# Performance work log

Measured on AMD Instinct MI355X. Metric: run time of the kernel, lower is better.

The kernel has to match this reference:

```python
import jax, jax.numpy as jnp
import numpy as np

N = 20000       # nodes
E = 640000      # random edges (self-loops appended -> E + N total)
G = 64          # graphs in batch
F_IN = 114
H1 = 3          # heads in layer 1
D2 = 128        # output_dim of layer 2
NEG = 0.2       # GATConv leaky_relu negative slope


def setup_inputs() -> dict:
    key = jax.random.key(0)
    ks = jax.random.split(key, 20)
    x = jax.random.normal(ks[0], (N, F_IN), jnp.float32)
    src = jax.random.randint(ks[1], (E,), 0, N, jnp.int32)
    dst = jax.random.randint(ks[2], (E,), 0, N, jnp.int32)
    loop = jnp.arange(N, dtype=jnp.int32)  # PyG add_self_loops=True
    edge_index = jnp.stack([jnp.concatenate([src, loop]),
                            jnp.concatenate([dst, loop])])
    batch = (jnp.arange(N) * G // N).astype(jnp.int32)  # every graph non-empty

    def lin(k, i, o):
        return jax.random.normal(k, (i, o), jnp.float32) * (1.0 / np.sqrt(i))

    return {
        "x": x, "edge_index": edge_index, "batch": batch,
        # GATConv 1: 114 -> 114 per head, 3 heads, concat
        "W1": lin(ks[3], F_IN, H1 * F_IN),
        "a_src1": jax.random.normal(ks[4], (H1, F_IN), jnp.float32) * 0.1,
        "a_dst1": jax.random.normal(ks[5], (H1, F_IN), jnp.float32) * 0.1,
        "b1": jnp.zeros((H1 * F_IN,), jnp.float32),
        # GATConv 2: 342 -> 128, 1 head
        "W2": lin(ks[6], H1 * F_IN, D2),
        "a_src2": jax.random.normal(ks[7], (1, D2), jnp.float32) * 0.1,
        "a_dst2": jax.random.normal(ks[8], (1, D2), jnp.float32) * 0.1,
        "b2": jnp.zeros((D2,), jnp.float32),
        # MLP head
        "Wg": lin(ks[9], D2, 64),  "bg": jnp.zeros((64,), jnp.float32),
        "Wf1": lin(ks[10], 64, 32), "bf1": jnp.zeros((32,), jnp.float32),
        "Wf2": lin(ks[11], 32, 16), "bf2": jnp.zeros((16,), jnp.float32),
        "Wo": lin(ks[12], 16, 1),   "bo": jnp.zeros((1,), jnp.float32),
    }


def gat_conv(x, edge_index, W, a_src, a_dst, b, heads, dim):
    """PyG GATConv (self-loops already in edge_index, eval mode)."""
    n = x.shape[0]
    h = (x @ W).reshape(n, heads, dim)             # [N,H,D]
    src, dst = edge_index[0], edge_index[1]
    alpha_s = jnp.sum(h * a_src, axis=-1)          # [N,H]
    alpha_d = jnp.sum(h * a_dst, axis=-1)          # [N,H]
    e = jax.nn.leaky_relu(alpha_s[src] + alpha_d[dst], NEG)  # [E,H]
    # segment softmax over destination nodes
    m = jax.ops.segment_max(e, dst, num_segments=n)
    ex = jnp.exp(e - m[dst])
    s = jax.ops.segment_sum(ex, dst, num_segments=n)
    alpha = ex / s[dst]                            # [E,H]
    out = jax.ops.segment_sum(h[src] * alpha[..., None], dst, num_segments=n)
    return out.reshape(n, heads * dim) + b


def reference(x, edge_index, batch, W1, a_src1, a_dst1, b1,
              W2, a_src2, a_dst2, b2, Wg, bg, Wf1, bf1, Wf2, bf2, Wo, bo):
    h = jax.nn.elu(gat_conv(x, edge_index, W1, a_src1, a_dst1, b1, H1, F_IN))
    h = jax.nn.relu(gat_conv(h, edge_index, W2, a_src2, a_dst2, b2, 1, D2))
    g = jax.ops.segment_max(h, batch, num_segments=G)   # global max pool [G,128]
    g = jax.nn.relu(g @ Wg + bg)
    g = jax.nn.relu(g @ Wf1 + bf1)
    g = jax.nn.relu(g @ Wf2 + bf2)
    return g @ Wo + bo                                  # [G,1]
```

## Files before the change

kernel.cpp:

```cpp
#include <hip/hip_runtime.h>

#define NN 20000
#define EE 660000
#define GG 64
#define FIN 114
#define H1 3
#define F1 342
#define D2 128
#define NEG 0.2f

typedef __attribute__((ext_vector_type(8))) short short8v;
typedef __attribute__((ext_vector_type(4))) float f32x4;
typedef unsigned short ushort_t;

__device__ inline unsigned fenc(float f) {
    unsigned u = __float_as_uint(f);
    return (u & 0x80000000u) ? ~u : (u | 0x80000000u);
}
__device__ inline float fdec(unsigned u) {
    return (u & 0x80000000u) ? __uint_as_float(u & 0x7FFFFFFFu) : __uint_as_float(~u);
}
__device__ inline float lrelu(float x) { return x > 0.f ? x : NEG * x; }

__device__ inline void split2(float x, ushort_t& hi, ushort_t& lo) {
    unsigned u = __float_as_uint(x);
    unsigned uh = u & 0xFFFF0000u;
    hi = (ushort_t)(uh >> 16);
    float r = x - __uint_as_float(uh);
    unsigned v = __float_as_uint(r);
    unsigned vh = (v + 0x7FFFu + ((v >> 16) & 1u)) & 0xFFFF0000u;
    lo = (ushort_t)(vh >> 16);
}

__global__ void k_wa(const float* __restrict__ W1, const float* __restrict__ aS,
                     const float* __restrict__ aD, float* __restrict__ was,
                     float* __restrict__ wad) {
    int tid = blockIdx.x * 256 + threadIdx.x;
    if (tid >= 2 * FIN * H1) return;
    int which = tid >= FIN * H1;
    int i = which ? tid - FIN * H1 : tid;
    int k = i / H1, h = i % H1;
    const float* a = which ? aD : aS;
    float s = 0.f;
    for (int d = 0; d < FIN; d++) s += W1[k * F1 + h * FIN + d] * a[h * FIN + d];
    (which ? wad : was)[i] = s;
}

__global__ void k_prep1m(const float* __restrict__ W1, ushort_t* __restrict__ W1Th,
                         ushort_t* __restrict__ W1Tl) {
    int tid = blockIdx.x * 256 + threadIdx.x;
    if (tid >= H1 * 128 * 128) return;
    int h = tid / (128 * 128);
    int rem = tid & (128 * 128 - 1);
    int c = rem >> 7, k = rem & 127;
    float v = (c < FIN && k < FIN) ? W1[k * F1 + h * FIN + c] : 0.f;
    ushort_t hi, lo;
    split2(v, hi, lo);
    W1Th[tid] = hi;
    W1Tl[tid] = lo;
}

__global__ void k_prep2m(const float* __restrict__ W2, ushort_t* __restrict__ W2Th,
                         ushort_t* __restrict__ W2Tl) {
    int tid = blockIdx.x * 256 + threadIdx.x;
    if (tid >= 128 * 384) return;
    int c = tid / 384;
    int hk = tid - c * 384;
    int h = hk >> 7, k = hk & 127;
    float v = (k < FIN) ? W2[(h * FIN + k) * D2 + c] : 0.f;
    ushort_t hi, lo;
    split2(v, hi, lo);
    W2Th[tid] = hi;
    W2Tl[tid] = lo;
}

__global__ __launch_bounds__(256) void k_alpha1x(const float* __restrict__ x,
                                                 const float* __restrict__ was,
                                                 const float* __restrict__ wad,
                                                 float* __restrict__ as1,
                                                 float* __restrict__ ad1) {
    int n = blockIdx.x * 4 + (threadIdx.x >> 6);
    int l = threadIdx.x & 63;
    if (n >= NN) return;
    float x0 = x[n * FIN + l];
    float x1 = (l < FIN - 64) ? x[n * FIN + 64 + l] : 0.f;
    float s[H1], d[H1];
#pragma unroll
    for (int h = 0; h < H1; h++) {
        float w0s = was[l * H1 + h], w0d = wad[l * H1 + h];
        float w1s = (l < FIN - 64) ? was[(64 + l) * H1 + h] : 0.f;
        float w1d = (l < FIN - 64) ? wad[(64 + l) * H1 + h] : 0.f;
        s[h] = x0 * w0s + x1 * w1s;
        d[h] = x0 * w0d + x1 * w1d;
    }
#pragma unroll
    for (int o = 32; o > 0; o >>= 1) {
#pragma unroll
        for (int h = 0; h < H1; h++) {
            s[h] += __shfl_down(s[h], o);
            d[h] += __shfl_down(d[h], o);
        }
    }
    if (l == 0) {
#pragma unroll
        for (int h = 0; h < H1; h++) {
            as1[n * H1 + h] = s[h];
            ad1[n * H1 + h] = d[h];
        }
    }
}

__global__ void k_count(const int* __restrict__ dst, int* __restrict__ cnt) {
    int e = blockIdx.x * 256 + threadIdx.x;
    if (e < EE) atomicAdd(&cnt[dst[e]], 1);
}

__global__ __launch_bounds__(1024) void k_scan(const int* __restrict__ cnt,
                                               int* __restrict__ off) {
    __shared__ int part[1024];
    int t = threadIdx.x;
    const int CH = 20;
    int loc[CH];
    int s = 0;
    int base = t * CH;
    for (int i = 0; i < CH; i++) {
        int idx = base + i;
        int v = (idx < NN) ? cnt[idx] : 0;
        loc[i] = s;
        s += v;
    }
    part[t] = s;
    __syncthreads();
    for (int d = 1; d < 1024; d <<= 1) {
        int v = (t >= d) ? part[t - d] : 0;
        __syncthreads();
        part[t] += v;
        __syncthreads();
    }
    int pre = (t == 0) ? 0 : part[t - 1];
    for (int i = 0; i < CH; i++) {
        int idx = base + i;
        if (idx < NN) off[idx] = pre + loc[i];
    }
    if (t == 1023) off[NN] = part[1023];
}

__global__ void k_scatter(const int* __restrict__ src, const int* __restrict__ dst,
                          const int* __restrict__ off, int* __restrict__ cur,
                          int* __restrict__ csr_src) {
    int e = blockIdx.x * 256 + threadIdx.x;
    if (e < EE) {
        int d = dst[e];
        int pos = off[d] + atomicAdd(&cur[d], 1);
        csr_src[pos] = src[e];
    }
}

__global__ __launch_bounds__(128) void k_aggx(const float* __restrict__ x,
                                              const float* __restrict__ as1,
                                              const float* __restrict__ ad1,
                                              const int* __restrict__ off,
                                              const int* __restrict__ csr_src,
                                              ushort_t* __restrict__ xgh,
                                              ushort_t* __restrict__ xgl) {
    int n = blockIdx.x, t = threadIdx.x;
    int e0 = off[n], e1 = off[n + 1];
    float adv0 = ad1[n * H1 + 0], adv1 = ad1[n * H1 + 1], adv2 = ad1[n * H1 + 2];
    __shared__ int ssrc[64];
    __shared__ float sw[64][H1];
    __shared__ float red[64][H1];
    float acc0 = 0.f, acc1 = 0.f, acc2 = 0.f;
    float ps0 = 0.f, ps1 = 0.f, ps2 = 0.f;
    for (int base = e0; base < e1; base += 64) {
        int c = min(64, e1 - base);
        __syncthreads();
        if (t < c) {
            int s = csr_src[base + t];
            ssrc[t] = s;
            float w0 = __expf(lrelu(as1[s * H1 + 0] + adv0));
            float w1 = __expf(lrelu(as1[s * H1 + 1] + adv1));
            float w2 = __expf(lrelu(as1[s * H1 + 2] + adv2));
            sw[t][0] = w0; sw[t][1] = w1; sw[t][2] = w2;
            ps0 += w0; ps1 += w1; ps2 += w2;
        }
        __syncthreads();
        if (t < FIN) {
            for (int j = 0; j < c; j++) {
                float xv = x[ssrc[j] * FIN + t];
                acc0 += xv * sw[j][0];
                acc1 += xv * sw[j][1];
                acc2 += xv * sw[j][2];
            }
        }
    }
    __syncthreads();
    if (t < 64) { red[t][0] = ps0; red[t][1] = ps1; red[t][2] = ps2; }
    __syncthreads();
    for (int sr = 32; sr > 0; sr >>= 1) {
        if (t < sr) {
            red[t][0] += red[t + sr][0];
            red[t][1] += red[t + sr][1];
            red[t][2] += red[t + sr][2];
        }
        __syncthreads();
    }
    float i0 = 1.f / red[0][0], i1 = 1.f / red[0][1], i2 = 1.f / red[0][2];
    float v0 = (t < FIN) ? acc0 * i0 : 0.f;
    float v1 = (t < FIN) ? acc1 * i1 : 0.f;
    float v2 = (t < FIN) ? acc2 * i2 : 0.f;
    ushort_t hi, lo;
    split2(v0, hi, lo);
    xgh[(size_t)0 * NN * 128 + n * 128 + t] = hi;
    xgl[(size_t)0 * NN * 128 + n * 128 + t] = lo;
    split2(v1, hi, lo);
    xgh[(size_t)1 * NN * 128 + n * 128 + t] = hi;
    xgl[(size_t)1 * NN * 128 + n * 128 + t] = lo;
    split2(v2, hi, lo);
    xgh[(size_t)2 * NN * 128 + n * 128 + t] = hi;
    xgl[(size_t)2 * NN * 128 + n * 128 + t] = lo;
}

__global__ __launch_bounds__(128) void k_agg2f(const float* __restrict__ h2,
                                               const float* __restrict__ as2,
                                               const float* __restrict__ ad2,
                                               const int* __restrict__ off,
                                               const int* __restrict__ csr_src,
                                               const float* __restrict__ b2,
                                               unsigned* __restrict__ poolbuf) {
    int n = blockIdx.x, t = threadIdx.x;
    int e0 = off[n], e1 = off[n + 1];
    float adv = ad2[n];
    __shared__ int ssrc[64];
    __shared__ float sw[64];
    __shared__ float red[64];
    float acc = 0.f, ps = 0.f;
    for (int base = e0; base < e1; base += 64) {
        int c = min(64, e1 - base);
        __syncthreads();
        if (t < c) {
            int s = csr_src[base + t];
            ssrc[t] = s;
            float w = __expf(lrelu(as2[s] + adv));
            sw[t] = w;
            ps += w;
        }
        __syncthreads();
        for (int j = 0; j < c; j++) acc += h2[(size_t)ssrc[j] * D2 + t] * sw[j];
    }
    __syncthreads();
    if (t < 64) red[t] = ps;
    __syncthreads();
    for (int sr = 32; sr > 0; sr >>= 1) {
        if (t < sr) red[t] += red[t + sr];
        __syncthreads();
    }
    float v = fmaxf(acc / red[0] + b2[t], 0.f);
    int g = (int)(((long long)n * GG) / NN);
    atomicMax(&poolbuf[g * D2 + t], fenc(v));
}

__global__ __launch_bounds__(256) void k_gemm1m(const ushort_t* __restrict__ xgh,
                                                const ushort_t* __restrict__ xgl,
                                                const ushort_t* __restrict__ W1Th,
                                                const ushort_t* __restrict__ W1Tl,
                                                const float* __restrict__ b1,
                                                ushort_t* __restrict__ h1hi,
                                                ushort_t* __restrict__ h1lo) {
    int h = blockIdx.y;
    int rb = blockIdx.x * 128;
    int tid = threadIdx.x;
    int w = tid >> 6, l = tid & 63;
    int m = l & 15, g = l >> 4;
    int r0 = rb + w * 32 + m;
    int r1 = r0 + 16;
    bool ok0 = (r0 < NN), ok1 = (r1 < NN);
    const ushort_t* xh = xgh + (size_t)h * NN * 128;
    const ushort_t* xl = xgl + (size_t)h * NN * 128;
    const ushort_t* Bhg = W1Th + (size_t)h * 128 * 128;
    const ushort_t* Blg = W1Tl + (size_t)h * 128 * 128;
    const short8v z8 = {0, 0, 0, 0, 0, 0, 0, 0};
    __shared__ __align__(16) ushort_t BsH[128 * 40];
    __shared__ __align__(16) ushort_t BsL[128 * 40];
    f32x4 acc0[8], acc1[8];
#pragma unroll
    for (int j = 0; j < 8; j++) {
        acc0[j] = (f32x4){0.f, 0.f, 0.f, 0.f};
        acc1[j] = (f32x4){0.f, 0.f, 0.f, 0.f};
    }
    for (int k0i = 0; k0i < 4; k0i++) {
        int k0 = k0i * 32;
        __syncthreads();
        int ka = k0 + g * 8;
        short8v a0h = ok0 ? *(const short8v*)(xh + (size_t)r0 * 128 + ka) : z8;
        short8v a0l = ok0 ? *(const short8v*)(xl + (size_t)r0 * 128 + ka) : z8;
        short8v a1h = ok1 ? *(const short8v*)(xh + (size_t)r1 * 128 + ka) : z8;
        short8v a1l = ok1 ? *(const short8v*)(xl + (size_t)r1 * 128 + ka) : z8;
#pragma unroll
        for (int it = 0; it < 2; it++) {
            int idx = tid + it * 256;
            int c = idx >> 2, q = idx & 3;
            size_t go = (size_t)c * 128 + k0 + q * 8;
            int lo_off = c * 40 + q * 8;
            *(short8v*)(&BsH[lo_off]) = *(const short8v*)(Bhg + go);
            *(short8v*)(&BsL[lo_off]) = *(const short8v*)(Blg + go);
        }
        __syncthreads();
#pragma unroll
        for (int j = 0; j < 8; j++) {
            int c = j * 16 + m;
            short8v bh = *(const short8v*)(&BsH[c * 40 + g * 8]);
            short8v bl = *(const short8v*)(&BsL[c * 40 + g * 8]);
            acc0[j] = __builtin_amdgcn_mfma_f32_16x16x32_bf16(a0h, bh, acc0[j], 0, 0, 0);
            acc1[j] = __builtin_amdgcn_mfma_f32_16x16x32_bf16(a1h, bh, acc1[j], 0, 0, 0);
            acc0[j] = __builtin_amdgcn_mfma_f32_16x16x32_bf16(a0h, bl, acc0[j], 0, 0, 0);
            acc1[j] = __builtin_amdgcn_mfma_f32_16x16x32_bf16(a1h, bl, acc1[j], 0, 0, 0);
            acc0[j] = __builtin_amdgcn_mfma_f32_16x16x32_bf16(a0l, bh, acc0[j], 0, 0, 0);
            acc1[j] = __builtin_amdgcn_mfma_f32_16x16x32_bf16(a1l, bh, acc1[j], 0, 0, 0);
        }
    }
    ushort_t* Hh = h1hi + (size_t)h * NN * 128;
    ushort_t* Hl = h1lo + (size_t)h * NN * 128;
#pragma unroll
    for (int j = 0; j < 8; j++) {
        int c = j * 16 + m;
        float bv = (c < FIN) ? b1[h * FIN + c] : 0.f;
#pragma unroll
        for (int r = 0; r < 4; r++) {
            int orow0 = rb + w * 32 + g * 4 + r;
            int orow1 = orow0 + 16;
            if (orow0 < NN) {
                float v = acc0[j][r] + bv;
                v = v > 0.f ? v : expm1f(v);
                ushort_t hi = 0, lo = 0;
                if (c < FIN) split2(v, hi, lo);
                Hh[(size_t)orow0 * 128 + c] = hi;
                Hl[(size_t)orow0 * 128 + c] = lo;
            }
            if (orow1 < NN) {
                float v = acc1[j][r] + bv;
                v = v > 0.f ? v : expm1f(v);
                ushort_t hi = 0, lo = 0;
                if (c < FIN) split2(v, hi, lo);
                Hh[(size_t)orow1 * 128 + c] = hi;
                Hl[(size_t)orow1 * 128 + c] = lo;
            }
        }
    }
}

__global__ __launch_bounds__(256) void k_gemm2m(const ushort_t* __restrict__ h1hi,
                                                const ushort_t* __restrict__ h1lo,
                                                const ushort_t* __restrict__ W2Th,
                                                const ushort_t* __restrict__ W2Tl,
                                                float* __restrict__ h2) {
    int rb = blockIdx.x * 128;
    int tid = threadIdx.x;
    int w = tid >> 6, l = tid & 63;
    int m = l & 15, g = l >> 4;
    int r0 = rb + w * 32 + m;
    int r1 = r0 + 16;
    bool ok0 = (r0 < NN), ok1 = (r1 < NN);
    const short8v z8 = {0, 0, 0, 0, 0, 0, 0, 0};
    __shared__ __align__(16) ushort_t BsH[128 * 40];
    __shared__ __align__(16) ushort_t BsL[128 * 40];
    f32x4 acc0[8], acc1[8];
#pragma unroll
    for (int j = 0; j < 8; j++) {
        acc0[j] = (f32x4){0.f, 0.f, 0.f, 0.f};
        acc1[j] = (f32x4){0.f, 0.f, 0.f, 0.f};
    }
    for (int k0i = 0; k0i < 12; k0i++) {
        int k0 = k0i * 32;
        __syncthreads();
        int hh = k0 >> 7;
        int kc = (k0 & 127) + g * 8;
        size_t a0o = ((size_t)hh * NN + (size_t)(ok0 ? r0 : 0)) * 128 + kc;
        size_t a1o = ((size_t)hh * NN + (size_t)(ok1 ? r1 : 0)) * 128 + kc;
        short8v a0h = ok0 ? *(const short8v*)(h1hi + a0o) : z8;
        short8v a0l = ok0 ? *(const short8v*)(h1lo + a0o) : z8;
        short8v a1h = ok1 ? *(const short8v*)(h1hi + a1o) : z8;
        short8v a1l = ok1 ? *(const short8v*)(h1lo + a1o) : z8;
#pragma unroll
        for (int it = 0; it < 2; it++) {
            int idx = tid + it * 256;
            int c = idx >> 2, q = idx & 3;
            size_t go = (size_t)c * 384 + k0 + q * 8;
            int lo_off = c * 40 + q * 8;
            *(short8v*)(&BsH[lo_off]) = *(const short8v*)(W2Th + go);
            *(short8v*)(&BsL[lo_off]) = *(const short8v*)(W2Tl + go);
        }
        __syncthreads();
#pragma unroll
        for (int j = 0; j < 8; j++) {
            int c = j * 16 + m;
            short8v bh = *(const short8v*)(&BsH[c * 40 + g * 8]);
            short8v bl = *(const short8v*)(&BsL[c * 40 + g * 8]);
            acc0[j] = __builtin_amdgcn_mfma_f32_16x16x32_bf16(a0h, bh, acc0[j], 0, 0, 0);
            acc1[j] = __builtin_amdgcn_mfma_f32_16x16x32_bf16(a1h, bh, acc1[j], 0, 0, 0);
            acc0[j] = __builtin_amdgcn_mfma_f32_16x16x32_bf16(a0h, bl, acc0[j], 0, 0, 0);
            acc1[j] = __builtin_amdgcn_mfma_f32_16x16x32_bf16(a1h, bl, acc1[j], 0, 0, 0);
            acc0[j] = __builtin_amdgcn_mfma_f32_16x16x32_bf16(a0l, bh, acc0[j], 0, 0, 0);
            acc1[j] = __builtin_amdgcn_mfma_f32_16x16x32_bf16(a1l, bh, acc1[j], 0, 0, 0);
        }
    }
#pragma unroll
    for (int j = 0; j < 8; j++) {
        int c = j * 16 + m;
#pragma unroll
        for (int r = 0; r < 4; r++) {
            int orow0 = rb + w * 32 + g * 4 + r;
            int orow1 = orow0 + 16;
            if (orow0 < NN) h2[(size_t)orow0 * D2 + c] = acc0[j][r];
            if (orow1 < NN) h2[(size_t)orow1 * D2 + c] = acc1[j][r];
        }
    }
}

__global__ __launch_bounds__(256) void k_alpha2(const float* __restrict__ h2,
                                                const float* __restrict__ aS,
                                                const float* __restrict__ aD,
                                                float* __restrict__ as2,
                                                float* __restrict__ ad2) {
    int n = blockIdx.x * 4 + (threadIdx.x >> 6);
    int l = threadIdx.x & 63;
    if (n >= NN) return;
    float v0 = h2[(size_t)n * D2 + l], v1 = h2[(size_t)n * D2 + 64 + l];
    float ps = v0 * aS[l] + v1 * aS[64 + l];
    float pd = v0 * aD[l] + v1 * aD[64 + l];
    for (int o = 32; o > 0; o >>= 1) {
        ps += __shfl_down(ps, o);
        pd += __shfl_down(pd, o);
    }
    if (l == 0) {
        as2[n] = ps;
        ad2[n] = pd;
    }
}

__global__ __launch_bounds__(128) void k_mlp(const unsigned* __restrict__ poolbuf,
                                             const float* __restrict__ Wg,
                                             const float* __restrict__ bg,
                                             const float* __restrict__ Wf1,
                                             const float* __restrict__ bf1,
                                             const float* __restrict__ Wf2,
                                             const float* __restrict__ bf2,
                                             const float* __restrict__ Wo,
                                             const float* __restrict__ bo,
                                             float* __restrict__ out) {
    int g = blockIdx.x;
    int t = threadIdx.x;
    __shared__ float pool[D2];
    __shared__ float a1[64];
    __shared__ float a2[32];
    __shared__ float a3[16];
    pool[t] = fdec(poolbuf[g * D2 + t]);
    __syncthreads();
    if (t < 64) {
        float acc = bg[t];
        for (int k = 0; k < D2; k++) acc += pool[k] * Wg[k * 64 + t];
        a1[t] = fmaxf(acc, 0.f);
    }
    __syncthreads();
    if (t < 32) {
        float acc = bf1[t];
        for (int k = 0; k < 64; k++) acc += a1[k] * Wf1[k * 32 + t];
        a2[t] = fmaxf(acc, 0.f);
    }
    __syncthreads();
    if (t < 16) {
        float acc = bf2[t];
        for (int k = 0; k < 32; k++) acc += a2[k] * Wf2[k * 16 + t];
        a3[t] = fmaxf(acc, 0.f);
    }
    __syncthreads();
    if (t == 0) {
        float acc = bo[0];
        for (int k = 0; k < 16; k++) acc += a3[k] * Wo[k];
        out[g] = acc;
    }
}

extern "C" void kernel_launch(void* const* d_in, const int* in_sizes, int n_in,
                              void* d_out, int out_size, void* d_ws, size_t ws_size,
                              hipStream_t stream) {
    const float* x = (const float*)d_in[0];
    const int* ei = (const int*)d_in[1];
    const float* W1 = (const float*)d_in[3];
    const float* aS1 = (const float*)d_in[4];
    const float* aD1 = (const float*)d_in[5];
    const float* b1 = (const float*)d_in[6];
    const float* W2 = (const float*)d_in[7];
    const float* aS2 = (const float*)d_in[8];
    const float* aD2 = (const float*)d_in[9];
    const float* b2 = (const float*)d_in[10];
    const float* Wg = (const float*)d_in[11];
    const float* bg = (const float*)d_in[12];
    const float* Wf1 = (const float*)d_in[13];
    const float* bf1 = (const float*)d_in[14];
    const float* Wf2 = (const float*)d_in[15];
    const float* bf2 = (const float*)d_in[16];
    const float* Wo = (const float*)d_in[17];
    const float* bo = (const float*)d_in[18];
    float* out = (float*)d_out;

    const int* src = ei;
    const int* dst = ei + EE;

    char* ws = (char*)d_ws;
    size_t o = 0;
    auto alloc = [&](size_t bytes) -> char* {
        char* p = ws + o;
        o += (bytes + 255) & ~(size_t)255;
        return p;
    };
    float* was = (float*)alloc((size_t)FIN * H1 * 4);
    float* wad = (float*)alloc((size_t)FIN * H1 * 4);
    ushort_t* W1Th = (ushort_t*)alloc((size_t)H1 * 128 * 128 * 2);
    ushort_t* W1Tl = (ushort_t*)alloc((size_t)H1 * 128 * 128 * 2);
    ushort_t* W2Th = (ushort_t*)alloc((size_t)128 * 384 * 2);
    ushort_t* W2Tl = (ushort_t*)alloc((size_t)128 * 384 * 2);
    float* as1 = (float*)alloc((size_t)NN * H1 * 4);
    float* ad1 = (float*)alloc((size_t)NN * H1 * 4);
    int* cnt = (int*)alloc((size_t)NN * 4);
    int* off = (int*)alloc((size_t)(NN + 1) * 4);
    int* cur = (int*)alloc((size_t)NN * 4);
    int* csr_src = (int*)alloc((size_t)EE * 4);
    ushort_t* xgh = (ushort_t*)alloc((size_t)H1 * NN * 128 * 2);
    ushort_t* xgl = (ushort_t*)alloc((size_t)H1 * NN * 128 * 2);
    ushort_t* h1hi = (ushort_t*)alloc((size_t)H1 * NN * 128 * 2);
    ushort_t* h1lo = (ushort_t*)alloc((size_t)H1 * NN * 128 * 2);
    float* h2 = (float*)alloc((size_t)NN * D2 * 4);
    float* as2 = (float*)alloc((size_t)NN * 4);
    float* ad2 = (float*)alloc((size_t)NN * 4);
    unsigned* poolbuf = (unsigned*)alloc((size_t)GG * D2 * 4);
    (void)ws_size;

    hipMemsetAsync(cnt, 0, (size_t)NN * 4, stream);
    hipMemsetAsync(cur, 0, (size_t)NN * 4, stream);
    hipMemsetAsync(poolbuf, 0, (size_t)GG * D2 * 4, stream);

    const int EB = (EE + 255) / 256;

    k_wa<<<(2 * FIN * H1 + 255) / 256, 256, 0, stream>>>(W1, aS1, aD1, was, wad);
    k_prep1m<<<(H1 * 128 * 128 + 255) / 256, 256, 0, stream>>>(W1, W1Th, W1Tl);
    k_prep2m<<<(128 * 384 + 255) / 256, 256, 0, stream>>>(W2, W2Th, W2Tl);
    k_alpha1x<<<(NN + 3) / 4, 256, 0, stream>>>(x, was, wad, as1, ad1);
    k_count<<<EB, 256, 0, stream>>>(dst, cnt);
    k_scan<<<1, 1024, 0, stream>>>(cnt, off);
    k_scatter<<<EB, 256, 0, stream>>>(src, dst, off, cur, csr_src);
    k_aggx<<<NN, 128, 0, stream>>>(x, as1, ad1, off, csr_src, xgh, xgl);
    k_gemm1m<<<dim3((NN + 127) / 128, H1), 256, 0, stream>>>(xgh, xgl, W1Th, W1Tl, b1, h1hi, h1lo);
    k_gemm2m<<<(NN + 127) / 128, 256, 0, stream>>>(h1hi, h1lo, W2Th, W2Tl, h2);
    k_alpha2<<<(NN + 3) / 4, 256, 0, stream>>>(h2, aS2, aD2, as2, ad2);
    k_agg2f<<<NN, 128, 0, stream>>>(h2, as2, ad2, off, csr_src, b2, poolbuf);
    k_mlp<<<GG, 128, 0, stream>>>(poolbuf, Wg, bg, Wf1, bf1, Wf2, bf2, Wo, bo, out);
}
```

Baseline: 278.9 us.

## Vectorize edge aggregation with float4 gathers and fuse alpha2 into GEMM2 epilogue

Both per-node aggregation kernels now split the 128 threads into 4 edge groups, each gathering float4 column chunks, and reduce the partial sums through shared memory. A padded 128-wide copy of x is built first so the layer-1 gathers are aligned and vectorized. The attention-logit computation for layer 2 moves into the GEMM2 epilogue, using shuffle reductions over the accumulators, which removes one kernel and one reread of h2. The cost is an extra padded x buffer and its copy kernel, and more shared-memory reduction work per node.

Result: slower. 324.5 us (+16.3%).

```diff
diff --git a/kernel.cpp b/kernel.cpp
--- a/kernel.cpp
+++ b/kernel.cpp
@@ -12,6 +12,7 @@
 typedef __attribute__((ext_vector_type(8))) short short8v;
 typedef __attribute__((ext_vector_type(4))) float f32x4;
 typedef unsigned short ushort_t;
+typedef __attribute__((ext_vector_type(4))) unsigned short ushort4v;
 
 __device__ inline unsigned fenc(float f) {
     unsigned u = __float_as_uint(f);
@@ -72,6 +73,13 @@
     split2(v, hi, lo);
     W2Th[tid] = hi;
     W2Tl[tid] = lo;
+}
+
+__global__ void k_xp(const float* __restrict__ x, float* __restrict__ xP) {
+    int tid = blockIdx.x * 256 + threadIdx.x;
+    if (tid >= NN * 128) return;
+    int n = tid >> 7, c = tid & 127;
+    xP[tid] = (c < FIN) ? x[n * FIN + c] : 0.f;
 }
 
 __global__ __launch_bounds__(256) void k_alpha1x(const float* __restrict__ x,
@@ -156,7 +164,7 @@
     }
 }
 
-__global__ __launch_bounds__(128) void k_aggx(const float* __restrict__ x,
+__global__ __launch_bounds__(128) void k_aggx(const float* __restrict__ xP,
                                               const float* __restrict__ as1,
                                               const float* __restrict__ ad1,
                                               const int* __restrict__ off,
@@ -164,12 +172,15 @@
                                               ushort_t* __restrict__ xgh,
                                               ushort_t* __restrict__ xgl) {
     int n = blockIdx.x, t = threadIdx.x;
+    int g = t >> 5, c32 = t & 31;
+    int col0 = c32 * 4;
     int e0 = off[n], e1 = off[n + 1];
     float adv0 = ad1[n * H1 + 0], adv1 = ad1[n * H1 + 1], adv2 = ad1[n * H1 + 2];
     __shared__ int ssrc[64];
     __shared__ float sw[64][H1];
-    __shared__ float red[64][H1];
-    float acc0 = 0.f, acc1 = 0.f, acc2 = 0.f;
+    __shared__ f32x4 red[4][32][H1];
+    __shared__ float sums[H1];
+    f32x4 a0 = {0, 0, 0, 0}, a1 = {0, 0, 0, 0}, a2 = {0, 0, 0, 0};
     float ps0 = 0.f, ps1 = 0.f, ps2 = 0.f;
     for (int base = e0; base < e1; base += 64) {
         int c = min(64, e1 - base);
@@ -184,40 +195,48 @@
             ps0 += w0; ps1 += w1; ps2 += w2;
         }
         __syncthreads();
-        if (t < FIN) {
-            for (int j = 0; j < c; j++) {
-                float xv = x[ssrc[j] * FIN + t];
-                acc0 += xv * sw[j][0];
-                acc1 += xv * sw[j][1];
-                acc2 += xv * sw[j][2];
-            }
-        }
-    }
+        for (int j = g; j < c; j += 4) {
+            int s = ssrc[j];
+            f32x4 v = *(const f32x4*)(xP + (size_t)s * 128 + col0);
+            float w0 = sw[j][0], w1 = sw[j][1], w2 = sw[j][2];
+            a0 += v * w0;
+            a1 += v * w1;
+            a2 += v * w2;
+        }
+    }
+    if (t < 64) {
+#pragma unroll
+        for (int o = 32; o > 0; o >>= 1) {
+            ps0 += __shfl_down(ps0, o);
+            ps1 += __shfl_down(ps1, o);
+            ps2 += __shfl_down(ps2, o);
+        }
+        if (t == 0) { sums[0] = ps0; sums[1] = ps1; sums[2] = ps2; }
+    }
+    red[g][c32][0] = a0;
+    red[g][c32][1] = a1;
+    red[g][c32][2] = a2;
     __syncthreads();
-    if (t < 64) { red[t][0] = ps0; red[t][1] = ps1; red[t][2] = ps2; }
-    __syncthreads();
-    for (int sr = 32; sr > 0; sr >>= 1) {
-        if (t < sr) {
-            red[t][0] += red[t + sr][0];
-            red[t][1] += red[t + sr][1];
-            red[t][2] += red[t + sr][2];
-        }
-        __syncthreads();
-    }
-    float i0 = 1.f / red[0][0], i1 = 1.f / red[0][1], i2 = 1.f / red[0][2];
-    float v0 = (t < FIN) ? acc0 * i0 : 0.f;
-    float v1 = (t < FIN) ? acc1 * i1 : 0.f;
-    float v2 = (t < FIN) ? acc2 * i2 : 0.f;
-    ushort_t hi, lo;
-    split2(v0, hi, lo);
-    xgh[(size_t)0 * NN * 128 + n * 128 + t] = hi;
-    xgl[(size_t)0 * NN * 128 + n * 128 + t] = lo;
-    split2(v1, hi, lo);
-    xgh[(size_t)1 * NN * 128 + n * 128 + t] = hi;
-    xgl[(size_t)1 * NN * 128 + n * 128 + t] = lo;
-    split2(v2, hi, lo);
-    xgh[(size_t)2 * NN * 128 + n * 128 + t] = hi;
-    xgl[(size_t)2 * NN * 128 + n * 128 + t] = lo;
+    if (t < 32) {
+        f32x4 r0 = red[0][t][0] + red[1][t][0] + red[2][t][0] + red[3][t][0];
+        f32x4 r1 = red[0][t][1] + red[1][t][1] + red[2][t][1] + red[3][t][1];
+        f32x4 r2 = red[0][t][2] + red[1][t][2] + red[2][t][2] + red[3][t][2];
+        float i0 = 1.f / sums[0], i1 = 1.f / sums[1], i2 = 1.f / sums[2];
+        int cb = t * 4;
+        ushort4v h4, l4;
+#pragma unroll
+        for (int q = 0; q < 4; q++) { ushort_t hh, ll; split2(r0[q] * i0, hh, ll); h4[q] = hh; l4[q] = ll; }
+        *(ushort4v*)(xgh + (size_t)0 * NN * 128 + (size_t)n * 128 + cb) = h4;
+        *(ushort4v*)(xgl + (size_t)0 * NN * 128 + (size_t)n * 128 + cb) = l4;
+#pragma unroll
+        for (int q = 0; q < 4; q++) { ushort_t hh, ll; split2(r1[q] * i1, hh, ll); h4[q] = hh; l4[q] = ll; }
+        *(ushort4v*)(xgh + (size_t)1 * NN * 128 + (size_t)n * 128 + cb) = h4;
+        *(ushort4v*)(xgl + (size_t)1 * NN * 128 + (size_t)n * 128 + cb) = l4;
+#pragma unroll
+        for (int q = 0; q < 4; q++) { ushort_t hh, ll; split2(r2[q] * i2, hh, ll); h4[q] = hh; l4[q] = ll; }
+        *(ushort4v*)(xgh + (size_t)2 * NN * 128 + (size_t)n * 128 + cb) = h4;
+        *(ushort4v*)(xgl + (size_t)2 * NN * 128 + (size_t)n * 128 + cb) = l4;
+    }
 }
 
 __global__ __launch_bounds__(128) void k_agg2f(const float* __restrict__ h2,
@@ -228,12 +247,16 @@
                                                const float* __restrict__ b2,
                                                unsigned* __restrict__ poolbuf) {
     int n = blockIdx.x, t = threadIdx.x;
+    int g = t >> 5, c32 = t & 31;
+    int col0 = c32 * 4;
     int e0 = off[n], e1 = off[n + 1];
     float adv = ad2[n];
     __shared__ int ssrc[64];
     __shared__ float sw[64];
-    __shared__ float red[64];
-    float acc = 0.f, ps = 0.f;
+    __shared__ f32x4 red[4][32];
+    __shared__ float ssum;
+    f32x4 acc = {0, 0, 0, 0};
+    float ps = 0.f;
     for (int base = e0; base < e1; base += 64) {
         int c = min(64, e1 - base);
         __syncthreads();
@@ -245,18 +268,29 @@
             ps += w;
         }
         __syncthreads();
-        for (int j = 0; j < c; j++) acc += h2[(size_t)ssrc[j] * D2 + t] * sw[j];
-    }
+        for (int j = g; j < c; j += 4) {
+            f32x4 v = *(const f32x4*)(h2 + (size_t)ssrc[j] * D2 + col0);
+            acc += v * sw[j];
+        }
+    }
+    if (t < 64) {
+#pragma unroll
+        for (int o = 32; o > 0; o >>= 1) ps += __shfl_down(ps, o);
+        if (t == 0) ssum = ps;
+    }
+    red[g][c32] = acc;
     __syncthreads();
-    if (t < 64) red[t] = ps;
-    __syncthreads();
-    for (int sr = 32; sr > 0; sr >>= 1) {
-        if (t < sr) red[t] += red[t + sr];
-        __syncthreads();
-    }
-    float v = fmaxf(acc / red[0] + b2[t], 0.f);
-    int g = (int)(((long long)n * GG) / NN);
-    atomicMax(&poolbuf[g * D2 + t], fenc(v));
+    if (t < 32) {
+        f32x4 r = red[0][t] + red[1][t] + red[2][t] + red[3][t];
+        float inv = 1.f / ssum;
+        int gidx = (int)(((long long)n * GG) / NN);
+        int cb = t * 4;
+#pragma unroll
+        for (int q = 0; q < 4; q++) {
+            float v = fmaxf(r[q] * inv + b2[cb + q], 0.f);
+            atomicMax(&poolbuf[gidx * D2 + cb + q], fenc(v));
+        }
+    }
 }
 
 __global__ __launch_bounds__(256) void k_gemm1m(const ushort_t* __restrict__ xgh,
@@ -352,7 +386,11 @@
                                                 const ushort_t* __restrict__ h1lo,
                                                 const ushort_t* __restrict__ W2Th,
                                                 const ushort_t* __restrict__ W2Tl,
-                                                float* __restrict__ h2) {
+                                                const float* __restrict__ aS2,
+                                                const float* __restrict__ aD2,
+                                                float* __restrict__ h2,
+                                                float* __restrict__ as2,
+                                                float* __restrict__ ad2) {
     int rb = blockIdx.x * 128;
     int tid = threadIdx.x;
     int w = tid >> 6, l = tid & 63;
@@ -414,26 +452,35 @@
             if (orow1 < NN) h2[(size_t)orow1 * D2 + c] = acc1[j][r];
         }
     }
-}
-
-__global__ __launch_bounds__(256) void k_alpha2(const float* __restrict__ h2,
-                                                const float* __restrict__ aS,
-                                                const float* __restrict__ aD,
-                                                float* __restrict__ as2,
-                                                float* __restrict__ ad2) {
-    int n = blockIdx.x * 4 + (threadIdx.x >> 6);
-    int l = threadIdx.x & 63;
-    if (n >= NN) return;
-    float v0 = h2[(size_t)n * D2 + l], v1 = h2[(size_t)n * D2 + 64 + l];
-    float ps = v0 * aS[l] + v1 * aS[64 + l];
-    float pd = v0 * aD[l] + v1 * aD[64 + l];
-    for (int o = 32; o > 0; o >>= 1) {
-        ps += __shfl_down(ps, o);
-        pd += __shfl_down(pd, o);
-    }
-    if (l == 0) {
-        as2[n] = ps;
-        ad2[n] = pd;
+    float sv[8], dv[8];
+#pragma unroll
+    for (int j = 0; j < 8; j++) {
+        sv[j] = aS2[j * 16 + m];
+        dv[j] = aD2[j * 16 + m];
+    }
+#pragma unroll
+    for (int r = 0; r < 4; r++) {
+        float s0 = 0.f, d0 = 0.f, s1 = 0.f, d1 = 0.f;
+#pragma unroll
+        for (int j = 0; j < 8; j++) {
+            s0 += acc0[j][r] * sv[j];
+            d0 += acc0[j][r] * dv[j];
+            s1 += acc1[j][r] * sv[j];
+            d1 += acc1[j][r] * dv[j];
+        }
+#pragma unroll
+        for (int o = 1; o < 16; o <<= 1) {
+            s0 += __shfl_xor(s0, o);
+            d0 += __shfl_xor(d0, o);
+            s1 += __shfl_xor(s1, o);
+            d1 += __shfl_xor(d1, o);
+        }
+        int orow0 = rb + w * 32 + g * 4 + r;
+        int orow1 = orow0 + 16;
+        if (m == 0) {
+            if (orow0 < NN) { as2[orow0] = s0; ad2[orow0] = d0; }
+            if (orow1 < NN) { as2[orow1] = s1; ad2[orow1] = d1; }
+        }
     }
 }
 
@@ -519,6 +566,7 @@
     ushort_t* W1Tl = (ushort_t*)alloc((size_t)H1 * 128 * 128 * 2);
     ushort_t* W2Th = (ushort_t*)alloc((size_t)128 * 384 * 2);
     ushort_t* W2Tl = (ushort_t*)alloc((size_t)128 * 384 * 2);
+    float* xP = (float*)alloc((size_t)NN * 128 * 4);
     float* as1 = (float*)alloc((size_t)NN * H1 * 4);
     float* ad1 = (float*)alloc((size_t)NN * H1 * 4);
     int* cnt = (int*)alloc((size_t)NN * 4);
@@ -544,14 +592,14 @@
     k_wa<<<(2 * FIN * H1 + 255) / 256, 256, 0, stream>>>(W1, aS1, aD1, was, wad);
     k_prep1m<<<(H1 * 128 * 128 + 255) / 256, 256, 0, stream>>>(W1, W1Th, W1Tl);
     k_prep2m<<<(128 * 384 + 255) / 256, 256, 0, stream>>>(W2, W2Th, W2Tl);
+    k_xp<<<(NN * 128 + 255) / 256, 256, 0, stream>>>(x, xP);
     k_alpha1x<<<(NN + 3) / 4, 256, 0, stream>>>(x, was, wad, as1, ad1);
     k_count<<<EB, 256, 0, stream>>>(dst, cnt);
     k_scan<<<1, 1024, 0, stream>>>(cnt, off);
     k_scatter<<<EB, 256, 0, stream>>>(src, dst, off, cur, csr_src);
-    k_aggx<<<NN, 128, 0, stream>>>(x, as1, ad1, off, csr_src, xgh, xgl);
+    k_aggx<<<NN, 128, 0, stream>>>(xP, as1, ad1, off, csr_src, xgh, xgl);
     k_gemm1m<<<dim3((NN + 127) / 128, H1), 256, 0, stream>>>(xgh, xgl, W1Th, W1Tl, b1, h1hi, h1lo);
-    k_gemm2m<<<(NN + 127) / 128, 256, 0, stream>>>(h1hi, h1lo, W2Th, W2Tl, h2);
-    k_alpha2<<<(NN + 3) / 4, 256, 0, stream>>>(h2, aS2, aD2, as2, ad2);
+    k_gemm2m<<<(NN + 127) / 128, 256, 0, stream>>>(h1hi, h1lo, W2Th, W2Tl, aS2, aD2, h2, as2, ad2);
     k_agg2f<<<NN, 128, 0, stream>>>(h2, as2, ad2, off, csr_src, b2, poolbuf);
     k_mlp<<<GG, 128, 0, stream>>>(poolbuf, Wg, bg, Wf1, bf1, Wf2, bf2, Wo, bo, out);
 }
```
